# Kernel optimization log

Measured on AMD Instinct MI355X. Metric: run time of the kernel, lower is better.

Reference implementation:

```python
import jax, jax.numpy as jnp
import numpy as np

V, D, NL, S, B = 32000, 1024, 2, 2048, 1
EXPAND, N, K = 2, 16, 4
DI = EXPAND * D
EPS = 1e-5


def setup_inputs() -> dict:
    key = jax.random.key(0)
    ks = jax.random.split(key, 10)
    std = 0.02
    inp = {
        "input_ids": jax.random.randint(ks[0], (B, S), 0, V),
        "embedding": jax.random.normal(ks[1], (V, D), jnp.float32) * std,
        "in_proj_w": jax.random.normal(ks[2], (NL, 2 * DI, D), jnp.float32) * std,
        "conv_w": jax.random.normal(ks[3], (NL, DI, 1, K), jnp.float32) * std,
        "conv_b": jnp.zeros((NL, DI), jnp.float32),
        "x_proj_w": jax.random.normal(ks[4], (NL, 2 * N, DI), jnp.float32) * std,
        "dt_proj_w": jax.random.normal(ks[5], (NL, DI, DI), jnp.float32) * std,
        "dt_proj_b": jnp.zeros((NL, DI), jnp.float32),
        "A_log": jnp.broadcast_to(jnp.log(jnp.arange(1, N + 1, dtype=jnp.float32)), (NL, DI, N)).copy(),
        "D_param": jnp.ones((NL, DI), jnp.float32),
        "out_proj_w": jax.random.normal(ks[6], (NL, D, DI), jnp.float32) * std,
        "norm_w": jnp.ones((NL, D), jnp.float32),
        "norm_f_w": jnp.ones((D,), jnp.float32),
        "lm_head_w": jax.random.normal(ks[7], (V, D), jnp.float32) * std,
    }
    return inp


def rmsnorm(x, w):
    rms = jnp.sqrt(jnp.mean(x * x, axis=-1, keepdims=True) + EPS)
    return x / rms * w


def silu(x):
    return x * jax.nn.sigmoid(x)


def ssm_layer(x, in_w, cw, cb, xp_w, dt_w, dt_b, A_log, Dp):
    b, s, _ = x.shape
    xz = jnp.einsum("bsd,ed->bse", x, in_w)  # (B,S,2*DI)
    xi, z = jnp.split(xz, 2, axis=-1)
    # depthwise causal conv1d
    xc = jnp.swapaxes(xi, 1, 2)  # (B,DI,S)
    xc = jax.lax.conv_general_dilated(
        xc, cw, window_strides=(1,), padding=[(K - 1, 0)],
        dimension_numbers=("NCH", "OIH", "NCH"), feature_group_count=DI,
    ) + cb[None, :, None]
    xi = silu(jnp.swapaxes(xc, 1, 2))  # (B,S,DI)
    bc = jnp.einsum("bsd,ed->bse", xi, xp_w)  # (B,S,2N)
    Bc, Cc = jnp.split(bc, 2, axis=-1)
    dt = jax.nn.softplus(jnp.einsum("bsd,ed->bse", xi, dt_w) + dt_b)
    A = -jnp.exp(A_log)  # (DI,N)
    dA = jnp.exp(dt[..., None] * A)                      # (B,S,DI,N)
    dBu = dt[..., None] * Bc[:, :, None, :] * xi[..., None]  # (B,S,DI,N)

    def step(h, t):
        dA_t, dBu_t, C_t, u_t = t
        h = dA_t * h + dBu_t                     # (B,DI,N)
        y = jnp.sum(h * C_t[:, None, :], axis=-1) + Dp * u_t  # (B,DI)
        return h, y

    xs = (jnp.swapaxes(dA, 0, 1), jnp.swapaxes(dBu, 0, 1),
          jnp.swapaxes(Cc, 0, 1), jnp.swapaxes(xi, 0, 1))
    h0 = jnp.zeros((b, DI, N), x.dtype)
    _, ys = jax.lax.scan(step, h0, xs)
    y = jnp.swapaxes(ys, 0, 1)  # (B,S,DI)
    y = y * silu(z)
    return y


def reference(input_ids, embedding, in_proj_w, conv_w, conv_b, x_proj_w,
              dt_proj_w, dt_proj_b, A_log, D_param, out_proj_w, norm_w,
              norm_f_w, lm_head_w):
    x = embedding[input_ids]  # (B,S,D)
    for l in range(NL):
        h = rmsnorm(x, norm_w[l])
        y = ssm_layer(h, in_proj_w[l], conv_w[l], conv_b[l], x_proj_w[l],
                      dt_proj_w[l], dt_proj_b[l], A_log[l], D_param[l])
        x = x + jnp.einsum("bse,de->bsd", y, out_proj_w[l])
    x = rmsnorm(x, norm_f_w)
    logits = jnp.einsum("bsd,vd->bsv", x, lm_head_w)
    return logits
```

## Files before the change

kernel.cpp:

```cpp
#include <hip/hip_runtime.h>
#include <hip/hip_bf16.h>
#include <stdint.h>
#include <stddef.h>

#define Vv   32000
#define Dd   1024
#define NLay 2
#define Ss   2048
#define Nn   16
#define Kc   4
#define DIc  2048
#define EPSf 1e-5f
#define LCH  32
#define NCHc (Ss / LCH)
#define CATR 2176

typedef __attribute__((ext_vector_type(8))) short bf16x8;
typedef __attribute__((ext_vector_type(4))) float f32x4;

__device__ __forceinline__ short f2bf(float f) {
  union { float f; unsigned u; } a; a.f = f;
  return (short)((a.u + 0x7FFFu + ((a.u >> 16) & 1u)) >> 16);
}
__device__ __forceinline__ float bf2f(short s) {
  union { unsigned u; float f; } a; a.u = ((unsigned)(unsigned short)s) << 16;
  return a.f;
}
__device__ __forceinline__ int hswz(int r) { return (r & 3) ^ ((r >> 2) & 3); }

struct CvtSeg { const float* s; short* d; unsigned n4; };
struct CvtBatch { CvtSeg seg[7]; unsigned tot4; };
__global__ __launch_bounds__(256) void cvt_all_k(CvtBatch b) {
  for (unsigned idx = blockIdx.x * 256 + threadIdx.x; idx < b.tot4;
       idx += gridDim.x * 256) {
    unsigned r = idx;
    int sg = 0;
    while (sg < 6 && r >= b.seg[sg].n4) { r -= b.seg[sg].n4; ++sg; }
    float4 v = ((const float4*)b.seg[sg].s)[r];
    short4 o;
    o.x = f2bf(v.x); o.y = f2bf(v.y); o.z = f2bf(v.z); o.w = f2bf(v.w);
    ((short4*)b.seg[sg].d)[r] = o;
  }
}

__global__ __launch_bounds__(256) void embed_k(const int* __restrict__ ids,
                                               const float* __restrict__ emb,
                                               float* __restrict__ x) {
  int s = blockIdx.x;
  int id = ids[s];
  const float4* src = (const float4*)(emb + (size_t)id * Dd);
  float4* dst = (float4*)(x + (size_t)s * Dd);
  dst[threadIdx.x] = src[threadIdx.x];
}

__global__ __launch_bounds__(256) void rmsnorm_k(const float* __restrict__ x,
                                                 const float* __restrict__ w,
                                                 short* __restrict__ o) {
  int s = blockIdx.x, t = threadIdx.x;
  float4 v = ((const float4*)(x + (size_t)s * Dd))[t];
  float ss = v.x * v.x + v.y * v.y + v.z * v.z + v.w * v.w;
#pragma unroll
  for (int off = 32; off; off >>= 1) ss += __shfl_down(ss, off);
  __shared__ float red[4];
  if ((t & 63) == 0) red[t >> 6] = ss;
  __syncthreads();
  ss = red[0] + red[1] + red[2] + red[3];
  float rinv = rsqrtf(ss * (1.0f / Dd) + EPSf);
  float4 wv = ((const float4*)w)[t];
  short4 ov;
  ov.x = f2bf(v.x * rinv * wv.x);
  ov.y = f2bf(v.y * rinv * wv.y);
  ov.z = f2bf(v.z * rinv * wv.z);
  ov.w = f2bf(v.w * rinv * wv.w);
  ((short4*)(o + (size_t)s * Dd))[t] = ov;
}

template <int BM, int BN, int WM, int WN, bool RESID, bool CAT>
__global__ __launch_bounds__(WM * WN * 64, 2) void gemm_ring(
    const short* __restrict__ A, const short* __restrict__ B,
    float* C, const float* resb, float* C2, int M, int N, int K, int nMt) {
  constexpr int NT = WM * WN * 64;
  constexpr int FM = BM / (WM * 16);
  constexpr int FN = BN / (WN * 16);
  constexpr int PA = BM * 4 / NT;
  constexpr int PB = BN * 4 / NT;
  static_assert(PA + PB == 4, "vmcnt literals assume 4 loads per stage");
  __shared__ short lds[4][(BM + BN) * 32];
  const int t = threadIdx.x;
  const int lane = t & 63;
  const int w = t >> 6;
  const int wm = w / WN, wn = w % WN;
  const int lr = lane & 15, l4 = lane >> 4;
  const int nwg = gridDim.x;
  const int chunk = nwg >> 3;
  const int wg = (blockIdx.x & 7) * chunk + (blockIdx.x >> 3);
  const int mi = wg % nMt, ni = wg / nMt;
  const size_t rowBase = (size_t)mi * BM, colBase = (size_t)ni * BN;

  const short* aSrc[PA]; int aOff[PA];
  const short* bSrc[PB]; int bOff[PB];
#pragma unroll
  for (int p = 0; p < PA; ++p) {
    int q = p * NT + t;
    int row = q >> 2, s = q & 3;
    aSrc[p] = A + (rowBase + row) * K + ((s ^ hswz(row)) << 3);
    aOff[p] = q * 8;
  }
#pragma unroll
  for (int p = 0; p < PB; ++p) {
    int q = p * NT + t;
    int row = q >> 2, s = q & 3;
    bSrc[p] = B + (colBase + row) * K + ((s ^ hswz(row)) << 3);
    bOff[p] = BM * 32 + q * 8;
  }
  auto stage = [&](int buf, int k0) {
#pragma unroll
    for (int p = 0; p < PA; ++p)
      __builtin_amdgcn_global_load_lds(
          (__attribute__((address_space(1))) unsigned int*)(aSrc[p] + k0),
          (__attribute__((address_space(3))) unsigned int*)(&lds[buf][aOff[p]]), 16, 0, 0);
#pragma unroll
    for (int p = 0; p < PB; ++p)
      __builtin_amdgcn_global_load_lds(
          (__attribute__((address_space(1))) unsigned int*)(bSrc[p] + k0),
          (__attribute__((address_space(3))) unsigned int*)(&lds[buf][bOff[p]]), 16, 0, 0);
  };

  f32x4 acc[FM][FN];
#pragma unroll
  for (int i = 0; i < FM; i++)
#pragma unroll
    for (int j = 0; j < FN; j++) acc[i][j] = f32x4{0.f, 0.f, 0.f, 0.f};

  const int KT = K >> 5;
  stage(0, 0); stage(1, 32); stage(2, 64);
  for (int kt = 0; kt < KT; ++kt) {
    const int rem = KT - 1 - kt;
    __builtin_amdgcn_sched_barrier(0);
    if (rem >= 2)      asm volatile("s_waitcnt vmcnt(8)" ::: "memory");
    else if (rem == 1) asm volatile("s_waitcnt vmcnt(4)" ::: "memory");
    else               asm volatile("s_waitcnt vmcnt(0)" ::: "memory");
    __builtin_amdgcn_sched_barrier(0);
    __builtin_amdgcn_s_barrier();
    __builtin_amdgcn_sched_barrier(0);
    if (kt + 3 < KT) stage((kt + 3) & 3, (kt + 3) << 5);
    const short* la = &lds[kt & 3][0];
    const short* lb = &lds[kt & 3][BM * 32];
    bf16x8 av[FM], bv[FN];
#pragma unroll
    for (int i = 0; i < FM; i++) {
      int r = wm * (FM * 16) + i * 16 + lr;
      av[i] = *(const bf16x8*)&la[r * 32 + ((l4 ^ hswz(r)) << 3)];
    }
#pragma unroll
    for (int j = 0; j < FN; j++) {
      int r = wn * (FN * 16) + j * 16 + lr;
      bv[j] = *(const bf16x8*)&lb[r * 32 + ((l4 ^ hswz(r)) << 3)];
    }
    __builtin_amdgcn_s_setprio(1);
#pragma unroll
    for (int i = 0; i < FM; i++)
#pragma unroll
      for (int j = 0; j < FN; j++)
        acc[i][j] = __builtin_amdgcn_mfma_f32_16x16x32_bf16(av[i], bv[j], acc[i][j], 0, 0, 0);
    __builtin_amdgcn_s_setprio(0);
  }
#pragma unroll
  for (int i = 0; i < FM; i++) {
#pragma unroll
    for (int j = 0; j < FN; j++) {
      size_t r0 = rowBase + wm * (FM * 16) + i * 16 + l4 * 4;
      size_t c = colBase + wn * (FN * 16) + j * 16 + lr;
#pragma unroll
      for (int rr = 0; rr < 4; rr++) {
        size_t r = r0 + rr;
        float v = acc[i][j][rr];
        if (CAT) {
          if (c < DIc) {
            float xv = v + resb[c];
            C[r * DIc + c] = fmaxf(xv, 0.f) + log1pf(__expf(-fabsf(xv)));
          } else if (c < DIc + 2 * Nn) {
            C2[r * (2 * Nn) + (c - DIc)] = v;
          }
        } else {
          size_t idx = r * N + c;
          if (RESID) v += resb[idx];
          C[idx] = v;
        }
      }
    }
  }
}

__global__ __launch_bounds__(256) void conv_silu_k(const float* __restrict__ xz,
                                                   const float* __restrict__ cw,
                                                   const float* __restrict__ cb,
                                                   short* __restrict__ xiC) {
  int idx = blockIdx.x * 256 + threadIdx.x;
  int s = idx / (DIc / 4), c4 = idx - s * (DIc / 4);
  const float4* xz4 = (const float4*)xz;
  const size_t rstride = 2 * DIc / 4;
  float4 zero = {0.f, 0.f, 0.f, 0.f};
  float4 x0 = (s >= 3) ? xz4[(size_t)(s - 3) * rstride + c4] : zero;
  float4 x1 = (s >= 2) ? xz4[(size_t)(s - 2) * rstride + c4] : zero;
  float4 x2 = (s >= 1) ? xz4[(size_t)(s - 1) * rstride + c4] : zero;
  float4 x3 = xz4[(size_t)s * rstride + c4];
  float4 cbv = ((const float4*)cb)[c4];
  short4 ov;
  float xs[4][4] = {{x0.x, x1.x, x2.x, x3.x}, {x0.y, x1.y, x2.y, x3.y},
                    {x0.z, x1.z, x2.z, x3.z}, {x0.w, x1.w, x2.w, x3.w}};
  float cbs[4] = {cbv.x, cbv.y, cbv.z, cbv.w};
  short os[4];
#pragma unroll
  for (int j = 0; j < 4; j++) {
    float4 wv = ((const float4*)cw)[c4 * 4 + j];
    float acc = cbs[j] + wv.x * xs[j][0] + wv.y * xs[j][1] + wv.z * xs[j][2] + wv.w * xs[j][3];
    os[j] = f2bf(acc / (1.f + __expf(-acc)));
  }
  ov.x = os[0]; ov.y = os[1]; ov.z = os[2]; ov.w = os[3];
  ((short4*)xiC)[idx] = ov;
}

__global__ __launch_bounds__(256) void scan_pass1(const float* __restrict__ dt,
                                                  const short* __restrict__ u,
                                                  const float* __restrict__ bc,
                                                  const float* __restrict__ alog,
                                                  float* __restrict__ Ap,
                                                  float* __restrict__ Hl) {
  const int j = blockIdx.x;
  const int d = blockIdx.y * 256 + threadIdx.x;
  __shared__ float sB[LCH][Nn];
  for (int q = threadIdx.x; q < LCH * Nn; q += 256) {
    int tt = q >> 4, n = q & 15;
    sB[tt][n] = bc[(size_t)(j * LCH + tt) * 32 + n];
  }
  __syncthreads();
  float Ar[Nn], h[Nn], ap[Nn];
#pragma unroll
  for (int n = 0; n < Nn; n++) {
    Ar[n] = -__expf(alog[d * Nn + n]); h[n] = 0.f; ap[n] = 1.f;
  }
  const int t0 = j * LCH;
  for (int tt = 0; tt < LCH; tt++) {
    size_t gi = (size_t)(t0 + tt) * DIc + d;
    float dtv = dt[gi];
    float uv = bf2f(u[gi]);
    float dtu = dtv * uv;
#pragma unroll
    for (int n = 0; n < Nn; n++) {
      float a = __expf(dtv * Ar[n]);
      h[n] = a * h[n] + dtu * sB[tt][n];
      ap[n] *= a;
    }
  }
  size_t base = ((size_t)j * DIc + d) * Nn;
#pragma unroll
  for (int n = 0; n < Nn; n++) { Ap[base + n] = ap[n]; Hl[base + n] = h[n]; }
}

__global__ __launch_bounds__(256) void scan_combine(const float* __restrict__ Ap,
                                                    const float* __restrict__ Hl,
                                                    float* __restrict__ Hi) {
  int idx = blockIdx.x * 256 + threadIdx.x;
  float h = 0.f;
  for (int j = 0; j < NCHc; j++) {
    size_t o = (size_t)j * DIc * Nn + idx;
    Hi[o] = h;
    h = Ap[o] * h + Hl[o];
  }
}

__global__ __launch_bounds__(256) void scan_pass2(const float* __restrict__ dt,
                                                  const short* __restrict__ u,
                                                  const float* __restrict__ bc,
                                                  const float* __restrict__ alog,
                                                  const float* __restrict__ Hinit,
                                                  const float* __restrict__ Dp,
                                                  const float* __restrict__ xz,
                                                  short* __restrict__ y) {
  const int j = blockIdx.x;
  const int d = blockIdx.y * 256 + threadIdx.x;
  __shared__ float sB[LCH][Nn], sC[LCH][Nn];
  for (int q = threadIdx.x; q < LCH * Nn; q += 256) {
    int tt = q >> 4, n = q & 15;
    size_t r = (size_t)(j * LCH + tt) * 32;
    sB[tt][n] = bc[r + n];
    sC[tt][n] = bc[r + 16 + n];
  }
  __syncthreads();
  float Ar[Nn], h[Nn];
  size_t hb = ((size_t)j * DIc + d) * Nn;
#pragma unroll
  for (int n = 0; n < Nn; n++) {
    Ar[n] = -__expf(alog[d * Nn + n]); h[n] = Hinit[hb + n];
  }
  float dp = Dp[d];
  const int t0 = j * LCH;
  for (int tt = 0; tt < LCH; tt++) {
    size_t gi = (size_t)(t0 + tt) * DIc + d;
    float dtv = dt[gi];
    float uv = bf2f(u[gi]);
    float dtu = dtv * uv;
    float yv = dp * uv;
#pragma unroll
    for (int n = 0; n < Nn; n++) {
      float a = __expf(dtv * Ar[n]);
      h[n] = a * h[n] + dtu * sB[tt][n];
      yv += h[n] * sC[tt][n];
    }
    float zv = xz[(size_t)(t0 + tt) * (2 * DIc) + DIc + d];
    float sz = zv / (1.f + __expf(-zv));
    y[gi] = f2bf(yv * sz);
  }
}

extern "C" void kernel_launch(void* const* d_in, const int* in_sizes, int n_in,
                              void* d_out, int out_size, void* d_ws, size_t ws_size,
                              hipStream_t stream) {
  (void)in_sizes; (void)n_in; (void)out_size; (void)ws_size;
  const int* ids = (const int*)d_in[0];
  const float* emb = (const float*)d_in[1];
  const float* in_proj_w = (const float*)d_in[2];
  const float* conv_w = (const float*)d_in[3];
  const float* conv_b = (const float*)d_in[4];
  const float* x_proj_w = (const float*)d_in[5];
  const float* dt_proj_w = (const float*)d_in[6];
  const float* dt_proj_b = (const float*)d_in[7];
  const float* A_log = (const float*)d_in[8];
  const float* D_param = (const float*)d_in[9];
  const float* out_proj_w = (const float*)d_in[10];
  const float* norm_w = (const float*)d_in[11];
  const float* norm_f_w = (const float*)d_in[12];
  const float* lm_head_w = (const float*)d_in[13];
  float* logits = (float*)d_out;

  char* ws = (char*)d_ws;
  size_t woff = 0;
  auto walloc = [&](size_t bytes) { void* p = ws + woff; woff += (bytes + 255) & ~(size_t)255; return p; };
  float* x     = (float*)walloc((size_t)Ss * Dd * 4);
  short* xfbf  = (short*)walloc((size_t)Ss * Dd * 2);
  short* w_lm  = (short*)walloc((size_t)Vv * Dd * 2);

  char* sc = (char*)d_out;
  size_t soff = 0;
  auto salloc = [&](size_t bytes) { void* p = sc + soff; soff += (bytes + 255) & ~(size_t)255; return p; };
  float* xz   = (float*)salloc((size_t)Ss * 2 * DIc * 4);
  float* dtb  = (float*)salloc((size_t)Ss * DIc * 4);
  float* bc   = (float*)salloc((size_t)Ss * 32 * 4);
  float* Ap   = (float*)salloc((size_t)NCHc * DIc * Nn * 4);
  float* Hl   = (float*)salloc((size_t)NCHc * DIc * Nn * 4);
  float* Hi   = (float*)salloc((size_t)NCHc * DIc * Nn * 4);
  short* hbf  = (short*)salloc((size_t)Ss * Dd * 2);
  short* xiC  = (short*)salloc((size_t)Ss * DIc * 2);
  short* ybf  = (short*)salloc((size_t)Ss * DIc * 2);
  short* w_in = (short*)salloc((size_t)NLay * 2 * DIc * Dd * 2);
  short* w_cat= (short*)salloc((size_t)NLay * CATR * DIc * 2);
  short* w_out= (short*)salloc((size_t)NLay * Dd * DIc * 2);

  CvtBatch cb2{};
  unsigned tot = 0;
  auto addseg = [&](int i, const float* s, short* d, size_t n) {
    cb2.seg[i].s = s; cb2.seg[i].d = d; cb2.seg[i].n4 = (unsigned)(n / 4);
    tot += (unsigned)(n / 4);
  };
  addseg(0, in_proj_w, w_in, (size_t)NLay * 2 * DIc * Dd);
  addseg(1, out_proj_w, w_out, (size_t)NLay * Dd * DIc);
  addseg(2, lm_head_w, w_lm, (size_t)Vv * Dd);
  addseg(3, dt_proj_w, w_cat, (size_t)DIc * DIc);
  addseg(4, x_proj_w, w_cat + (size_t)DIc * DIc, (size_t)2 * Nn * DIc);
  addseg(5, dt_proj_w + (size_t)DIc * DIc, w_cat + (size_t)CATR * DIc, (size_t)DIc * DIc);
  addseg(6, x_proj_w + (size_t)2 * Nn * DIc,
         w_cat + (size_t)CATR * DIc + (size_t)DIc * DIc, (size_t)2 * Nn * DIc);
  cb2.tot4 = tot;
  cvt_all_k<<<dim3(4096), dim3(256), 0, stream>>>(cb2);

  embed_k<<<dim3(Ss), dim3(256), 0, stream>>>(ids, emb, x);

  for (int l = 0; l < NLay; l++) {
    rmsnorm_k<<<dim3(Ss), dim3(256), 0, stream>>>(x, norm_w + (size_t)l * Dd, hbf);
    gemm_ring<128, 128, 2, 2, false, false><<<dim3(512), dim3(256), 0, stream>>>(
        hbf, w_in + (size_t)l * 2 * DIc * Dd, xz, nullptr, nullptr, Ss, 2 * DIc, Dd, 16);
    conv_silu_k<<<dim3(Ss * DIc / 4 / 256), dim3(256), 0, stream>>>(
        xz, conv_w + (size_t)l * DIc * Kc, conv_b + (size_t)l * DIc, xiC);
    gemm_ring<128, 128, 2, 2, false, true><<<dim3(272), dim3(256), 0, stream>>>(
        xiC, w_cat + (size_t)l * CATR * DIc, dtb, dt_proj_b + (size_t)l * DIc, bc,
        Ss, CATR, DIc, 16);
    scan_pass1<<<dim3(NCHc, DIc / 256), dim3(256), 0, stream>>>(
        dtb, xiC, bc, A_log + (size_t)l * DIc * Nn, Ap, Hl);
    scan_combine<<<dim3(DIc * Nn / 256), dim3(256), 0, stream>>>(Ap, Hl, Hi);
    scan_pass2<<<dim3(NCHc, DIc / 256), dim3(256), 0, stream>>>(
        dtb, xiC, bc, A_log + (size_t)l * DIc * Nn, Hi,
        D_param + (size_t)l * DIc, xz, ybf);
    gemm_ring<128, 128, 2, 2, true, false><<<dim3(128), dim3(256), 0, stream>>>(
        ybf, w_out + (size_t)l * Dd * DIc, x, x, nullptr, Ss, Dd, DIc, 16);
  }

  rmsnorm_k<<<dim3(Ss), dim3(256), 0, stream>>>(x, norm_f_w, xfbf);
  gemm_ring<256, 256, 2, 4, false, false><<<dim3(1000), dim3(512), 0, stream>>>(
      xfbf, w_lm, logits, nullptr, nullptr, Ss, Vv, Dd, 8);
}
```

Before: 659.7 us.

## Add dedicated 256x256 LM-head GEMM with direct-to-LDS loads and fuse embed+rmsnorm

Replaces the generic ring GEMM for the LM head with a specialized 256x256 tile kernel. It loads A and B straight into XOR-swizzled LDS with global_load_lds, double-buffers, issues the next stage's loads after the fragment reads, and raises wave priority around the MFMA blocks. It also fuses the embedding gather with the first layer's RMSNorm, saving one launch and one read of x. The new GEMM assumes M, N and K divide the tile sizes and that the grid divides by 8, and it drops the generic kernel's bounds handling.

Measured after the change: 644.1 us, median of 2. -2.4%, faster.

```diff
diff --git a/kernel.cpp b/kernel.cpp
--- a/kernel.cpp
+++ b/kernel.cpp
@@ -43,14 +43,30 @@
   }
 }
 
-__global__ __launch_bounds__(256) void embed_k(const int* __restrict__ ids,
-                                               const float* __restrict__ emb,
-                                               float* __restrict__ x) {
-  int s = blockIdx.x;
+__global__ __launch_bounds__(256) void embed_norm_k(const int* __restrict__ ids,
+                                                    const float* __restrict__ emb,
+                                                    const float* __restrict__ w,
+                                                    float* __restrict__ x,
+                                                    short* __restrict__ o) {
+  int s = blockIdx.x, t = threadIdx.x;
   int id = ids[s];
-  const float4* src = (const float4*)(emb + (size_t)id * Dd);
-  float4* dst = (float4*)(x + (size_t)s * Dd);
-  dst[threadIdx.x] = src[threadIdx.x];
+  float4 v = ((const float4*)(emb + (size_t)id * Dd))[t];
+  ((float4*)(x + (size_t)s * Dd))[t] = v;
+  float ss = v.x * v.x + v.y * v.y + v.z * v.z + v.w * v.w;
+#pragma unroll
+  for (int off = 32; off; off >>= 1) ss += __shfl_down(ss, off);
+  __shared__ float red[4];
+  if ((t & 63) == 0) red[t >> 6] = ss;
+  __syncthreads();
+  ss = red[0] + red[1] + red[2] + red[3];
+  float rinv = rsqrtf(ss * (1.0f / Dd) + EPSf);
+  float4 wv = ((const float4*)w)[t];
+  short4 ov;
+  ov.x = f2bf(v.x * rinv * wv.x);
+  ov.y = f2bf(v.y * rinv * wv.y);
+  ov.z = f2bf(v.z * rinv * wv.z);
+  ov.w = f2bf(v.w * rinv * wv.w);
+  ((short4*)(o + (size_t)s * Dd))[t] = ov;
 }
 
 __global__ __launch_bounds__(256) void rmsnorm_k(const float* __restrict__ x,
@@ -192,6 +208,116 @@
   }
 }
 
+__global__ __launch_bounds__(512, 2) void gemm256(const short* __restrict__ A,
+                                                  const short* __restrict__ B,
+                                                  float* __restrict__ C,
+                                                  int M, int N, int K, int nMt) {
+  __shared__ short lds[2][2][256 * 64];
+  const int t = threadIdx.x;
+  const int lane = t & 63;
+  const int w = t >> 6;
+  const int wm = w >> 2, wn = w & 3;
+  const int lr = lane & 15, l4 = lane >> 4;
+  const int nwg = gridDim.x;
+  const int chunk = nwg >> 3;
+  const int wg = (blockIdx.x & 7) * chunk + (blockIdx.x >> 3);
+  const int mi = wg % nMt, ni = wg / nMt;
+  const size_t rowBase = (size_t)mi * 256, colBase = (size_t)ni * 256;
+
+  const short* aSrc[4]; const short* bSrc[4];
+  int ldsOff[4];
+#pragma unroll
+  for (int p = 0; p < 4; ++p) {
+    int q = p * 512 + t;
+    int row = q >> 3, s = q & 7;
+    int ks = (s ^ (row & 7)) * 8;
+    aSrc[p] = A + (rowBase + row) * K + ks;
+    bSrc[p] = B + (colBase + row) * K + ks;
+    ldsOff[p] = q * 8;
+  }
+  auto stage = [&](int buf, int k0) {
+#pragma unroll
+    for (int p = 0; p < 4; ++p)
+      __builtin_amdgcn_global_load_lds(
+          (__attribute__((address_space(1))) unsigned int*)(aSrc[p] + k0),
+          (__attribute__((address_space(3))) unsigned int*)(&lds[buf][0][ldsOff[p]]), 16, 0, 0);
+#pragma unroll
+    for (int p = 0; p < 4; ++p)
+      __builtin_amdgcn_global_load_lds(
+          (__attribute__((address_space(1))) unsigned int*)(bSrc[p] + k0),
+          (__attribute__((address_space(3))) unsigned int*)(&lds[buf][1][ldsOff[p]]), 16, 0, 0);
+  };
+
+  f32x4 acc[8][4];
+#pragma unroll
+  for (int i = 0; i < 8; i++)
+#pragma unroll
+    for (int j = 0; j < 4; j++) acc[i][j] = f32x4{0.f, 0.f, 0.f, 0.f};
+
+  stage(0, 0);
+  const int KT = K >> 6;
+  for (int kt = 0; kt < KT; ++kt) {
+    const int cur = kt & 1;
+    __syncthreads();
+    bf16x8 a0[4][2], b0[4][2];
+#pragma unroll
+    for (int i = 0; i < 4; i++)
+#pragma unroll
+      for (int kq = 0; kq < 2; kq++) {
+        int r = wm * 128 + i * 16 + lr;
+        int ks = kq * 4 + l4;
+        a0[i][kq] = *(const bf16x8*)&lds[cur][0][r * 64 + ((ks ^ (r & 7)) << 3)];
+      }
+#pragma unroll
+    for (int j = 0; j < 4; j++)
+#pragma unroll
+      for (int kq = 0; kq < 2; kq++) {
+        int r = wn * 64 + j * 16 + lr;
+        int ks = kq * 4 + l4;
+        b0[j][kq] = *(const bf16x8*)&lds[cur][1][r * 64 + ((ks ^ (r & 7)) << 3)];
+      }
+    if (kt + 1 < KT) stage(cur ^ 1, (kt + 1) << 6);
+    __builtin_amdgcn_s_setprio(1);
+#pragma unroll
+    for (int i = 0; i < 4; i++)
+#pragma unroll
+      for (int j = 0; j < 4; j++)
+#pragma unroll
+        for (int kq = 0; kq < 2; kq++)
+          acc[i][j] = __builtin_amdgcn_mfma_f32_16x16x32_bf16(a0[i][kq], b0[j][kq], acc[i][j], 0, 0, 0);
+    __builtin_amdgcn_s_setprio(0);
+    bf16x8 a1[4][2];
+#pragma unroll
+    for (int i = 0; i < 4; i++)
+#pragma unroll
+      for (int kq = 0; kq < 2; kq++) {
+        int r = wm * 128 + 64 + i * 16 + lr;
+        int ks = kq * 4 + l4;
+        a1[i][kq] = *(const bf16x8*)&lds[cur][0][r * 64 + ((ks ^ (r & 7)) << 3)];
+      }
+    __builtin_amdgcn_s_setprio(1);
+#pragma unroll
+    for (int i = 0; i < 4; i++)
+#pragma unroll
+      for (int j = 0; j < 4; j++)
+#pragma unroll
+        for (int kq = 0; kq < 2; kq++)
+          acc[i + 4][j] = __builtin_amdgcn_mfma_f32_16x16x32_bf16(a1[i][kq], b0[j][kq], acc[i + 4][j], 0, 0, 0);
+    __builtin_amdgcn_s_setprio(0);
+  }
+#pragma unroll
+  for (int i = 0; i < 8; i++) {
+#pragma unroll
+    for (int j = 0; j < 4; j++) {
+      size_t r0 = rowBase + wm * 128 + i * 16 + l4 * 4;
+      size_t c = colBase + wn * 64 + j * 16 + lr;
+#pragma unroll
+      for (int rr = 0; rr < 4; rr++)
+        C[(r0 + rr) * N + c] = acc[i][j][rr];
+    }
+  }
+}
+
 __global__ __launch_bounds__(256) void conv_silu_k(const float* __restrict__ xz,
                                                    const float* __restrict__ cw,
                                                    const float* __restrict__ cb,
@@ -374,10 +500,11 @@
   cb2.tot4 = tot;
   cvt_all_k<<<dim3(4096), dim3(256), 0, stream>>>(cb2);
 
-  embed_k<<<dim3(Ss), dim3(256), 0, stream>>>(ids, emb, x);
+  embed_norm_k<<<dim3(Ss), dim3(256), 0, stream>>>(ids, emb, norm_w, x, hbf);
 
   for (int l = 0; l < NLay; l++) {
-    rmsnorm_k<<<dim3(Ss), dim3(256), 0, stream>>>(x, norm_w + (size_t)l * Dd, hbf);
+    if (l > 0)
+      rmsnorm_k<<<dim3(Ss), dim3(256), 0, stream>>>(x, norm_w + (size_t)l * Dd, hbf);
     gemm_ring<128, 128, 2, 2, false, false><<<dim3(512), dim3(256), 0, stream>>>(
         hbf, w_in + (size_t)l * 2 * DIc * Dd, xz, nullptr, nullptr, Ss, 2 * DIc, Dd, 16);
     conv_silu_k<<<dim3(Ss * DIc / 4 / 256), dim3(256), 0, stream>>>(
@@ -396,6 +523,5 @@
   }
 
   rmsnorm_k<<<dim3(Ss), dim3(256), 0, stream>>>(x, norm_f_w, xfbf);
-  gemm_ring<256, 256, 2, 4, false, false><<<dim3(1000), dim3(512), 0, stream>>>(
-      xfbf, w_lm, logits, nullptr, nullptr, Ss, Vv, Dd, 8);
-}
+  gemm256<<<dim3(1000), dim3(512), 0, stream>>>(xfbf, w_lm, logits, Ss, Vv, Dd, 8);
+}
```
